# Kernel optimization log

Hardware: AMD Instinct MI355X
Metric: run time of the kernel (lower is better)

## Reference

```python
import jax, jax.numpy as jnp
import numpy as np

ALPHA = 0.5  # trapezoidal_alpha

def rmsnorm(x, w, eps=1e-5):
    return x * jax.lax.rsqrt(jnp.mean(x * x, axis=-1, keepdims=True) + eps) * w

def ssd_scan(x, Bc, Cc, dt, A, alpha):
    # x: (B,L,H,P), Bc/Cc: (B,L,N), dt: (B,L,H), A: (H,)
    da = jnp.exp(dt * A)  # (B,L,H), A < 0 so da in (0,1)
    shift = lambda t: jnp.concatenate([jnp.zeros_like(t[:, :1]), t[:, :-1]], axis=1)
    xp, bp, dtp = shift(x), shift(Bc), shift(dt)
    to_t = lambda t: jnp.moveaxis(t, 1, 0)
    xs = tuple(map(to_t, (x, Bc, Cc, dt, da, xp, bp, dtp)))
    Bb, _, H, P = x.shape
    N = Bc.shape[-1]
    h0 = jnp.zeros((Bb, H, P, N), x.dtype)
    def step(h, inp):
        xt, bt, ct, dtt, dat, xpt, bpt, dtpt = inp
        u = dtt[:, :, None, None] * xt[..., None] * bt[:, None, None, :]      # (B,H,P,N)
        up = dtpt[:, :, None, None] * xpt[..., None] * bpt[:, None, None, :]  # prev input term
        h = dat[:, :, None, None] * (h + alpha * up) + (1.0 - alpha) * u      # trapezoidal update
        y = jnp.einsum('bhpn,bn->bhp', h, ct)
        return h, y
    _, ys = jax.lax.scan(step, h0, xs)
    return jnp.moveaxis(ys, 0, 1)  # (B,L,H,P)

def setup_inputs() -> dict:
    key = jax.random.key(0)
    ks = jax.random.split(key, 10)
    B, NV, NQ = 4, 256, 32
    D, DI, H, N, E, NL = 1024, 2048, 32, 128, 1536, 12
    PROJ = 2 * DI + 2 * N + H  # z | x | B | C | dt
    s = 0.02
    return {
        'visual_tokens': jax.random.normal(ks[0], (B, NV, D), jnp.float32),
        'query_embeds': jax.random.normal(ks[1], (B, NQ, D), jnp.float32),
        'vis_w': jax.random.normal(ks[2], (D, D), jnp.float32) * s,
        'vis_b': jnp.zeros((D,), jnp.float32),
        'qry_w': jax.random.normal(ks[3], (D, D), jnp.float32) * s,
        'qry_b': jnp.zeros((D,), jnp.float32),
        'norm_ws': jnp.ones((NL, D), jnp.float32),
        'in_ws': jax.random.normal(ks[4], (NL, D, PROJ), jnp.float32) * s,
        'dt_biases': jax.random.normal(ks[5], (NL, H), jnp.float32) * 0.5,
        'A_logs': jnp.log(jnp.tile(jnp.arange(1.0, H + 1.0, dtype=jnp.float32)[None], (NL, 1))),
        'D_ssm': jnp.ones((NL, H), jnp.float32),
        'gnorm_ws': jnp.ones((NL, DI), jnp.float32),
        'out_ws': jax.random.normal(ks[6], (NL, DI, D), jnp.float32) * s,
        'norm_f_w': jnp.ones((D,), jnp.float32),
        'head_w': jax.random.normal(ks[7], (D, E), jnp.float32) * s,
        'head_b': jnp.zeros((E,), jnp.float32),
    }

def reference(visual_tokens, query_embeds, vis_w, vis_b, qry_w, qry_b, norm_ws, in_ws,
              dt_biases, A_logs, D_ssm, gnorm_ws, out_ws, norm_f_w, head_w, head_b):
    vis = visual_tokens @ vis_w + vis_b
    qry = query_embeds @ qry_w + qry_b
    hidden = jnp.concatenate([vis, qry], axis=1)  # (B,L,D)
    n_layers = in_ws.shape[0]
    d_inner = gnorm_ws.shape[-1]
    H = A_logs.shape[-1]
    P = d_inner // H
    N = (in_ws.shape[-1] - 2 * d_inner - H) // 2
    for i in range(n_layers):
        res = hidden
        xin = rmsnorm(hidden, norm_ws[i])
        proj = xin @ in_ws[i]  # (B,L,2*DI+2*N+H)
        z = proj[..., :d_inner]
        xss = proj[..., d_inner:2 * d_inner]
        Bc = proj[..., 2 * d_inner:2 * d_inner + N]
        Cc = proj[..., 2 * d_inner + N:2 * d_inner + 2 * N]
        dt = jax.nn.softplus(proj[..., 2 * d_inner + 2 * N:] + dt_biases[i])
        A = -jnp.exp(A_logs[i])
        xr = xss.reshape(xss.shape[0], xss.shape[1], H, P)
        y = ssd_scan(xr, Bc, Cc, dt, A, ALPHA) + D_ssm[i][None, None, :, None] * xr
        y = y.reshape(xss.shape)
        y = rmsnorm(y * jax.nn.silu(z), gnorm_ws[i])  # gated RMSNorm
        hidden = res + y @ out_ws[i]
    hidden = rmsnorm(hidden, norm_f_w)
    pooled = hidden.mean(axis=1)                   # (B,D)
    out = pooled @ head_w + head_b                 # (B,E)
    nrm = jnp.linalg.norm(out, axis=-1, keepdims=True)
    return out / jnp.maximum(nrm, 1e-12)           # F.normalize semantics
```

## Files before the change

kernel.cpp:

```cpp
#include <hip/hip_runtime.h>
#include <cmath>

#define Bb   4
#define Tt   288
#define Dd   1024
#define DIi  2048
#define HH   32
#define PP   64
#define NNs  128
#define PROJ  4384
#define PROJP 4480
#define NLl  12
#define EE   1536

typedef __bf16 bf16x8 __attribute__((ext_vector_type(8)));
typedef float f32x4 __attribute__((ext_vector_type(4)));
typedef float f32x16 __attribute__((ext_vector_type(16)));

__device__ __forceinline__ unsigned short f2bf(float v) {
  __bf16 b = (__bf16)v;
  return __builtin_bit_cast(unsigned short, b);
}
__device__ __forceinline__ float bf2f(unsigned short u) {
  unsigned int x = ((unsigned int)u) << 16;
  return __builtin_bit_cast(float, x);
}
__device__ __forceinline__ void split2(float v, unsigned short& h, unsigned short& l) {
  h = f2bf(v);
  l = f2bf(v - bf2f(h));
}

__device__ __forceinline__ void async16(const void* g, void* l) {
  __builtin_amdgcn_global_load_lds(
      (const __attribute__((address_space(1))) unsigned int*)g,
      (__attribute__((address_space(3))) unsigned int*)l, 16, 0, 0);
}

__device__ inline float block_reduce_sum(float v, float* lds) {
#pragma unroll
  for (int d = 32; d > 0; d >>= 1) v += __shfl_down(v, d, 64);
  int lane = threadIdx.x & 63;
  int w = threadIdx.x >> 6;
  if (lane == 0) lds[w] = v;
  __syncthreads();
  if (threadIdx.x == 0) {
    float s = lds[0];
    int nw = blockDim.x >> 6;
    for (int i = 1; i < nw; i++) s += lds[i];
    lds[0] = s;
  }
  __syncthreads();
  return lds[0];
}

__global__ __launch_bounds__(256) void cvt_act_k(const float* __restrict__ vis,
                                                 const float* __restrict__ qry,
                                                 unsigned short* __restrict__ oh,
                                                 unsigned short* __restrict__ ol) {
  int idx = (blockIdx.x * 256 + threadIdx.x) * 4;
  const float* src = (idx < 1024 * 1024) ? &vis[idx] : &qry[idx - 1024 * 1024];
  float4 v = *(const float4*)src;
  ushort4 h, l;
  split2(v.x, h.x, l.x); split2(v.y, h.y, l.y);
  split2(v.z, h.z, l.z); split2(v.w, h.w, l.w);
  *(ushort4*)&oh[idx] = h;
  *(ushort4*)&ol[idx] = l;
}

__global__ __launch_bounds__(256) void cvt_tr2_k(const float* __restrict__ W,
                                                 unsigned short* __restrict__ Wth,
                                                 unsigned short* __restrict__ Wtl,
                                                 int K, int N,
                                                 size_t wstride, size_t ostride) {
  __shared__ float tile[32][33];
  W   += (size_t)blockIdx.z * wstride;
  Wth += (size_t)blockIdx.z * ostride;
  Wtl += (size_t)blockIdx.z * ostride;
  const int n0 = blockIdx.x * 32, k0 = blockIdx.y * 32;
  const int c = threadIdx.x & 31;
  const int r0 = threadIdx.x >> 5;
#pragma unroll
  for (int j = 0; j < 4; j++) {
    int r = r0 + j * 8;
    int n = n0 + c;
    tile[r][c] = (n < N) ? W[(size_t)(k0 + r) * N + n] : 0.f;
  }
  __syncthreads();
  const int nl = threadIdx.x >> 3;
  const int kl = (threadIdx.x & 7) * 4;
  ushort4 h, l;
  split2(tile[kl + 0][nl], h.x, l.x);
  split2(tile[kl + 1][nl], h.y, l.y);
  split2(tile[kl + 2][nl], h.z, l.z);
  split2(tile[kl + 3][nl], h.w, l.w);
  size_t o = (size_t)(n0 + nl) * K + k0 + kl;
  *(ushort4*)&Wth[o] = h;
  *(ushort4*)&Wtl[o] = l;
}

template<int BM, int BN>
__global__ __launch_bounds__(256) void gemm3_k(
    const unsigned short* __restrict__ Ah, const unsigned short* __restrict__ Al,
    const unsigned short* __restrict__ Wh, const unsigned short* __restrict__ Wl,
    const float* __restrict__ bias, const float* __restrict__ res,
    float* __restrict__ C, int M, int N, int K,
    int rows_per_b, int T_total, int t_off)
{
  constexpr int FM = BM / 64;
  constexpr int FN = BN / 64;
  __shared__ __align__(16) unsigned short Ash[BM * 32];
  __shared__ __align__(16) unsigned short Asl[BM * 32];
  __shared__ __align__(16) unsigned short Bsh[BN * 32];
  __shared__ __align__(16) unsigned short Bsl[BN * 32];
  const int tid = threadIdx.x;
  const int lane = tid & 63;
  const int wm = (tid >> 6) >> 1;
  const int wn = (tid >> 6) & 1;
  const int m0 = blockIdx.y * BM;
  const int n0 = blockIdx.x * BN;
  const int lrow = lane & 31;
  const int lkb = (lane >> 5) * 8;

  f32x16 acc[FM][FN];
#pragma unroll
  for (int i = 0; i < FM; i++)
#pragma unroll
    for (int j = 0; j < FN; j++) acc[i][j] = (f32x16)0.0f;

  for (int k0 = 0; k0 < K; k0 += 32) {
#pragma unroll
    for (int c = 0; c < BM / 64; c++) {
      int o = (c * 256 + tid) * 16;
      int row = o >> 6;
      int colb = o & 63;
      size_t gb = ((size_t)(m0 + row) * K + k0) * 2 + colb;
      async16((const char*)Ah + gb, (char*)Ash + o);
      async16((const char*)Al + gb, (char*)Asl + o);
    }
#pragma unroll
    for (int c = 0; c < BN / 64; c++) {
      int o = (c * 256 + tid) * 16;
      int row = o >> 6;
      int colb = o & 63;
      size_t gb = ((size_t)(n0 + row) * K + k0) * 2 + colb;
      async16((const char*)Wh + gb, (char*)Bsh + o);
      async16((const char*)Wl + gb, (char*)Bsl + o);
    }
    __syncthreads();

#pragma unroll
    for (int kh = 0; kh < 2; kh++) {
      bf16x8 ah[FM], al[FM], bh[FN], bl[FN];
#pragma unroll
      for (int i = 0; i < FM; i++) {
        int off = (wm * (BM / 2) + i * 32 + lrow) * 32 + kh * 16 + lkb;
        ah[i] = *(const bf16x8*)&Ash[off];
        al[i] = *(const bf16x8*)&Asl[off];
      }
#pragma unroll
      for (int j = 0; j < FN; j++) {
        int off = (wn * (BN / 2) + j * 32 + lrow) * 32 + kh * 16 + lkb;
        bh[j] = *(const bf16x8*)&Bsh[off];
        bl[j] = *(const bf16x8*)&Bsl[off];
      }
#pragma unroll
      for (int i = 0; i < FM; i++)
#pragma unroll
        for (int j = 0; j < FN; j++) {
          acc[i][j] = __builtin_amdgcn_mfma_f32_32x32x16_bf16(ah[i], bh[j], acc[i][j], 0, 0, 0);
          acc[i][j] = __builtin_amdgcn_mfma_f32_32x32x16_bf16(ah[i], bl[j], acc[i][j], 0, 0, 0);
          acc[i][j] = __builtin_amdgcn_mfma_f32_32x32x16_bf16(al[i], bh[j], acc[i][j], 0, 0, 0);
        }
    }
    __syncthreads();
  }

  const int r0 = (lane >> 5) * 4;
#pragma unroll
  for (int i = 0; i < FM; i++) {
#pragma unroll
    for (int j = 0; j < FN; j++) {
      int ncol = n0 + wn * (BN / 2) + j * 32 + lrow;
      float bv = bias ? bias[ncol] : 0.f;
#pragma unroll
      for (int rg = 0; rg < 16; rg++) {
        int m = m0 + wm * (BM / 2) + i * 32 + (rg & 3) + 8 * (rg >> 2) + r0;
        size_t orow;
        if (T_total) {
          int bbv = m / rows_per_b;
          orow = (size_t)bbv * T_total + (m - bbv * rows_per_b) + t_off;
        } else {
          orow = (size_t)m;
        }
        float v = acc[i][j][rg] + bv;
        if (res) v += res[orow * N + ncol];
        C[orow * N + ncol] = v;
      }
    }
  }
}

__global__ __launch_bounds__(256) void gemm_k(
    const float* __restrict__ A, const float* __restrict__ W,
    const float* __restrict__ bias, const float* __restrict__ res,
    float* __restrict__ C, int M, int N, int K,
    int rows_per_b, int T_total, int t_off)
{
  __shared__ float As[16][64];
  __shared__ float Ws[16][64];
  const int tid = threadIdx.x;
  const int tx = tid & 15;
  const int ty = tid >> 4;
  const int m0 = blockIdx.y * 64;
  const int n0 = blockIdx.x * 64;
  float acc[4][4] = {};
  const int ar = tid >> 2;
  const int ac = (tid & 3) << 2;
  const int wr = tid >> 4;
  const int wc = (tid & 15) << 2;

  for (int k0 = 0; k0 < K; k0 += 16) {
    float4 av = {0.f, 0.f, 0.f, 0.f};
    int gr = m0 + ar;
    if (gr < M) av = *(const float4*)&A[(size_t)gr * K + k0 + ac];
    As[ac + 0][ar] = av.x; As[ac + 1][ar] = av.y;
    As[ac + 2][ar] = av.z; As[ac + 3][ar] = av.w;

    float4 wv = {0.f, 0.f, 0.f, 0.f};
    int gc = n0 + wc;
    const float* wp = &W[(size_t)(k0 + wr) * N + gc];
    if (gc + 3 < N) {
      wv = *(const float4*)wp;
    } else {
      if (gc + 0 < N) wv.x = wp[0];
      if (gc + 1 < N) wv.y = wp[1];
      if (gc + 2 < N) wv.z = wp[2];
    }
    *(float4*)&Ws[wr][wc] = wv;
    __syncthreads();
#pragma unroll
    for (int kk = 0; kk < 16; kk++) {
      float4 a4 = *(const float4*)&As[kk][ty << 2];
      float4 b4 = *(const float4*)&Ws[kk][tx << 2];
      float a[4] = {a4.x, a4.y, a4.z, a4.w};
      float b[4] = {b4.x, b4.y, b4.z, b4.w};
#pragma unroll
      for (int i = 0; i < 4; i++)
#pragma unroll
        for (int j = 0; j < 4; j++)
          acc[i][j] = fmaf(a[i], b[j], acc[i][j]);
    }
    __syncthreads();
  }
#pragma unroll
  for (int i = 0; i < 4; i++) {
    int gr = m0 + (ty << 2) + i;
    if (gr >= M) continue;
    int bbv = gr / rows_per_b;
    int tt = gr - bbv * rows_per_b;
    size_t orow = (size_t)bbv * T_total + tt + t_off;
#pragma unroll
    for (int j = 0; j < 4; j++) {
      int gc = n0 + (tx << 2) + j;
      if (gc >= N) continue;
      float v = acc[i][j];
      if (bias) v += bias[gc];
      if (res)  v += res[orow * (size_t)N + gc];
      C[orow * (size_t)N + gc] = v;
    }
  }
}

__global__ __launch_bounds__(256) void rmsnorm_k(
    const float* __restrict__ x, const float* __restrict__ w, float* __restrict__ out)
{
  __shared__ float lds[8];
  const int row = blockIdx.x;
  const float* xr = x + (size_t)row * Dd;
  float4 v = *(const float4*)&xr[threadIdx.x << 2];
  float ss = v.x * v.x + v.y * v.y + v.z * v.z + v.w * v.w;
  ss = block_reduce_sum(ss, lds);
  float sc = rsqrtf(ss * (1.f / Dd) + 1e-5f);
  float4 wv = *(const float4*)&w[threadIdx.x << 2];
  float4 o = {v.x * sc * wv.x, v.y * sc * wv.y, v.z * sc * wv.z, v.w * sc * wv.w};
  *(float4*)&out[(size_t)row * Dd + (threadIdx.x << 2)] = o;
}

__global__ __launch_bounds__(256) void rmsnorm2_k(
    const float* __restrict__ x, const float* __restrict__ w,
    unsigned short* __restrict__ oh, unsigned short* __restrict__ ol)
{
  __shared__ float lds[8];
  const int row = blockIdx.x;
  const float* xr = x + (size_t)row * Dd;
  float4 v = *(const float4*)&xr[threadIdx.x << 2];
  float ss = v.x * v.x + v.y * v.y + v.z * v.z + v.w * v.w;
  ss = block_reduce_sum(ss, lds);
  float sc = rsqrtf(ss * (1.f / Dd) + 1e-5f);
  float4 wv = *(const float4*)&w[threadIdx.x << 2];
  ushort4 h, l;
  split2(v.x * sc * wv.x, h.x, l.x);
  split2(v.y * sc * wv.y, h.y, l.y);
  split2(v.z * sc * wv.z, h.z, l.z);
  split2(v.w * sc * wv.w, h.w, l.w);
  size_t o = (size_t)row * Dd + (threadIdx.x << 2);
  *(ushort4*)&oh[o] = h;
  *(ushort4*)&ol[o] = l;
}

__global__ __launch_bounds__(64) void dtcum_k(
    const float* __restrict__ proj, const float* __restrict__ dt_bias,
    const float* __restrict__ A_log,
    float* __restrict__ dtt, double* __restrict__ dcum)
{
  const int h = blockIdx.x & 31;
  const int b = blockIdx.x >> 5;
  const int lane = threadIdx.x;
  const float A = -expf(A_log[h]);
  const float bias = dt_bias[h];
  const int rowo = (b * HH + h) * Tt;
  double base = 0.0;
  for (int c = 0; c < (Tt + 63) / 64; c++) {
    int t = c * 64 + lane;
    float dt = 0.f;
    if (t < Tt) {
      float v = proj[(size_t)(b * Tt + t) * PROJP + 2 * DIi + 2 * NNs + h] + bias;
      dt = (v > 20.f) ? v : log1pf(expf(v));
    }
    double a = (double)(dt * A);
#pragma unroll
    for (int d = 1; d < 64; d <<= 1) {
      double o = __shfl_up(a, d, 64);
      if (lane >= d) a += o;
    }
    double cum = base + a;
    if (t < Tt) { dtt[rowo + t] = dt; dcum[rowo + t] = cum; }
    base = __shfl(cum, 63, 64);
  }
}

__global__ __launch_bounds__(256) void cbgemm_k(const float* __restrict__ proj,
                                                float* __restrict__ St)
{
  const int tI = blockIdx.x, jI = blockIdx.y, b = blockIdx.z;
  if (jI > tI) return;
  __shared__ float Ct[32][130];
  __shared__ float Bt[32][130];
  const int tid = threadIdx.x;
  const int r = tid >> 3;
  const int q = (tid & 7) * 16;
  const float* pb = proj + (size_t)b * Tt * PROJP;
  {
    const float* crow = pb + (size_t)(tI * 32 + r) * PROJP + 2 * DIi + NNs + q;
    const float* brow = pb + (size_t)(jI * 32 + r) * PROJP + 2 * DIi + q;
#pragma unroll
    for (int f = 0; f < 16; f += 4) {
      float4 c4 = *(const float4*)&crow[f];
      float4 b4 = *(const float4*)&brow[f];
      *(float2*)&Ct[r][q + f]     = make_float2(c4.x, c4.y);
      *(float2*)&Ct[r][q + f + 2] = make_float2(c4.z, c4.w);
      *(float2*)&Bt[r][q + f]     = make_float2(b4.x, b4.y);
      *(float2*)&Bt[r][q + f + 2] = make_float2(b4.z, b4.w);
    }
  }
  __syncthreads();
  const int j_r = tid >> 3;
  const int t_c = (tid & 7) * 4;
  float acc[4] = {0.f, 0.f, 0.f, 0.f};
  for (int n = 0; n < NNs; n += 2) {
    float2 b2 = *(const float2*)&Bt[j_r][n];
#pragma unroll
    for (int k = 0; k < 4; k++) {
      float2 c2 = *(const float2*)&Ct[t_c + k][n];
      acc[k] = fmaf(b2.x, c2.x, acc[k]);
      acc[k] = fmaf(b2.y, c2.y, acc[k]);
    }
  }
  float* so = St + ((size_t)b * Tt + jI * 32 + j_r) * Tt + tI * 32 + t_c;
  *(float4*)so = make_float4(acc[0], acc[1], acc[2], acc[3]);
}

__global__ __launch_bounds__(256) void ssd_y_k(
    const float* __restrict__ proj, const float* __restrict__ St,
    const float* __restrict__ dtt, const double* __restrict__ dcum,
    const float* __restrict__ Dssm, float* __restrict__ ybuf)
{
  const int tI = blockIdx.x;
  const int h  = blockIdx.y;
  const int b  = blockIdx.z;
  __shared__ __align__(16) float Xs[32][64];
  __shared__ __align__(16) float Ss[32][36];
  __shared__ double cjs[32];
  const int tid = threadIdx.x;
  const int t_l = tid & 31;
  const int pg  = tid >> 5;
  const int t0  = tI * 32;
  const int rowo = (b * HH + h) * Tt;
  const double ct = dcum[rowo + t0 + t_l];
  const float Ds = Dssm[h];
  const float* pb = proj + (size_t)b * Tt * PROJP;
  float y[8] = {0,0,0,0,0,0,0,0};
  const int sr = tid >> 3;
  const int sq = tid & 7;

  for (int jI = 0; jI <= tI; jI++) {
    const int j0 = jI * 32;
    {
      const float* xr = pb + (size_t)(j0 + sr) * PROJP + DIi + h * PP + sq * 8;
      *(float4*)&Xs[sr][sq * 8]     = *(const float4*)&xr[0];
      *(float4*)&Xs[sr][sq * 8 + 4] = *(const float4*)&xr[4];
    }
    {
      const float* srow = St + ((size_t)b * Tt + j0 + sr) * Tt + t0 + sq * 4;
      float4 s4 = *(const float4*)srow;
      float dj = dtt[rowo + j0 + sr];
      s4.x *= dj; s4.y *= dj; s4.z *= dj; s4.w *= dj;
      *(float4*)&Ss[sr][sq * 4] = s4;
    }
    if (tid < 32) cjs[tid] = dcum[rowo + j0 + tid];
    __syncthreads();

    if (jI < tI) {
#pragma unroll 4
      for (int j = 0; j < 32; j++) {
        float d = (float)(ct - cjs[j]);
        float m = Ss[j][t_l] * expf(fminf(d, 0.f));
        const float* xp = &Xs[j][pg * 8];
        float4 a0 = *(const float4*)&xp[0];
        float4 a1 = *(const float4*)&xp[4];
        y[0] = fmaf(m, a0.x, y[0]); y[1] = fmaf(m, a0.y, y[1]);
        y[2] = fmaf(m, a0.z, y[2]); y[3] = fmaf(m, a0.w, y[3]);
        y[4] = fmaf(m, a1.x, y[4]); y[5] = fmaf(m, a1.y, y[5]);
        y[6] = fmaf(m, a1.z, y[6]); y[7] = fmaf(m, a1.w, y[7]);
      }
    } else {
      for (int j = 0; j < 32; j++) {
        float sv = Ss[j][t_l];
        float d = (float)(ct - cjs[j]);
        float m = sv * expf(fminf(d, 0.f));
        if (j == t_l) m = 0.5f * sv + Ds;
        if (j > t_l)  m = 0.f;
        const float* xp = &Xs[j][pg * 8];
        float4 a0 = *(const float4*)&xp[0];
        float4 a1 = *(const float4*)&xp[4];
        y[0] = fmaf(m, a0.x, y[0]); y[1] = fmaf(m, a0.y, y[1]);
        y[2] = fmaf(m, a0.z, y[2]); y[3] = fmaf(m, a0.w, y[3]);
        y[4] = fmaf(m, a1.x, y[4]); y[5] = fmaf(m, a1.y, y[5]);
        y[6] = fmaf(m, a1.z, y[6]); y[7] = fmaf(m, a1.w, y[7]);
      }
    }
    __syncthreads();
  }
  float* yo = &ybuf[(size_t)(b * Tt + t0 + t_l) * DIi + h * PP + pg * 8];
  *(float4*)&yo[0] = make_float4(y[0], y[1], y[2], y[3]);
  *(float4*)&yo[4] = make_float4(y[4], y[5], y[6], y[7]);
}

__global__ __launch_bounds__(256) void gate_norm2_k(
    const float* __restrict__ ybuf, const float* __restrict__ proj,
    const float* __restrict__ gw,
    unsigned short* __restrict__ yh, unsigned short* __restrict__ yl)
{
  __shared__ float lds[8];
  const int row = blockIdx.x;
  const float* yr = ybuf + (size_t)row * DIi;
  const float* zr = proj + (size_t)row * PROJP;
  const int base = threadIdx.x << 3;
  float4 z0 = *(const float4*)&zr[base];
  float4 z1 = *(const float4*)&zr[base + 4];
  float4 y0 = *(const float4*)&yr[base];
  float4 y1 = *(const float4*)&yr[base + 4];
  float zz[8] = {z0.x, z0.y, z0.z, z0.w, z1.x, z1.y, z1.z, z1.w};
  float yy[8] = {y0.x, y0.y, y0.z, y0.w, y1.x, y1.y, y1.z, y1.w};
  float g[8];
  float ss = 0.f;
#pragma unroll
  for (int e = 0; e < 8; e++) {
    float s = zz[e] / (1.f + expf(-zz[e]));
    float gv = yy[e] * s;
    g[e] = gv;
    ss += gv * gv;
  }
  ss = block_reduce_sum(ss, lds);
  float sc = rsqrtf(ss * (1.f / DIi) + 1e-5f);
  ushort4 h0, l0, h1, l1;
  split2(g[0] * sc * gw[base + 0], h0.x, l0.x);
  split2(g[1] * sc * gw[base + 1], h0.y, l0.y);
  split2(g[2] * sc * gw[base + 2], h0.z, l0.z);
  split2(g[3] * sc * gw[base + 3], h0.w, l0.w);
  split2(g[4] * sc * gw[base + 4], h1.x, l1.x);
  split2(g[5] * sc * gw[base + 5], h1.y, l1.y);
  split2(g[6] * sc * gw[base + 6], h1.z, l1.z);
  split2(g[7] * sc * gw[base + 7], h1.w, l1.w);
  size_t o = (size_t)row * DIi + base;
  *(ushort4*)&yh[o] = h0; *(ushort4*)&yh[o + 4] = h1;
  *(ushort4*)&yl[o] = l0; *(ushort4*)&yl[o + 4] = l1;
}

__global__ void pool_k(const float* __restrict__ xin, float* __restrict__ pooled) {
  int b = blockIdx.x;
  int d = blockIdx.y * 256 + threadIdx.x;
  const float* base = xin + (size_t)b * Tt * Dd + d;
  float s = 0.f;
  for (int t = 0; t < Tt; t++) s += base[(size_t)t * Dd];
  pooled[b * Dd + d] = s * (1.f / Tt);
}

__global__ __launch_bounds__(256) void l2norm_k(float* __restrict__ out) {
  __shared__ float lds[8];
  const int row = blockIdx.x;
  float* r = out + (size_t)row * EE;
  float v[6];
  float ss = 0.f;
#pragma unroll
  for (int e = 0; e < 6; e++) {
    v[e] = r[(e << 8) + threadIdx.x];
    ss += v[e] * v[e];
  }
  ss = block_reduce_sum(ss, lds);
  float sc = 1.f / fmaxf(sqrtf(ss), 1e-12f);
#pragma unroll
  for (int e = 0; e < 6; e++) r[(e << 8) + threadIdx.x] = v[e] * sc;
}

extern "C" void kernel_launch(void* const* d_in, const int* in_sizes, int n_in,
                              void* d_out, int out_size, void* d_ws, size_t ws_size,
                              hipStream_t stream) {
  (void)in_sizes; (void)n_in; (void)out_size;
  const float* visual   = (const float*)d_in[0];
  const float* query    = (const float*)d_in[1];
  const float* vis_w    = (const float*)d_in[2];
  const float* vis_b    = (const float*)d_in[3];
  const float* qry_w    = (const float*)d_in[4];
  const float* qry_b    = (const float*)d_in[5];
  const float* norm_ws  = (const float*)d_in[6];
  const float* in_ws    = (const float*)d_in[7];
  const float* dt_biases= (const float*)d_in[8];
  const float* A_logs   = (const float*)d_in[9];
  const float* D_ssm    = (const float*)d_in[10];
  const float* gnorm_ws = (const float*)d_in[11];
  const float* out_ws   = (const float*)d_in[12];
  const float* norm_f_w = (const float*)d_in[13];
  const float* head_w   = (const float*)d_in[14];
  const float* head_b   = (const float*)d_in[15];
  float* out = (float*)d_out;

  char* w = (char*)d_ws;
  float*          hidden = (float*)w;          w += (size_t)1152 * 1024 * 4;
  unsigned short* xh     = (unsigned short*)w; w += (size_t)1152 * 1024 * 2;
  unsigned short* xl     = (unsigned short*)w; w += (size_t)1152 * 1024 * 2;
  float*          proj   = (float*)w;          w += (size_t)1152 * PROJP * 4;
  float*          ybuf   = (float*)w;          w += (size_t)1152 * 2048 * 4;
  unsigned short* yh     = (unsigned short*)w; w += (size_t)1152 * 2048 * 2;
  unsigned short* yl     = (unsigned short*)w; w += (size_t)1152 * 2048 * 2;
  float*          dtt    = (float*)w;          w += (size_t)Bb * HH * Tt * 4;
  double*         dcum   = (double*)w;         w += (size_t)Bb * HH * Tt * 8;
  float*          Stb    = (float*)w;          w += (size_t)Bb * Tt * Tt * 4;
  float*          pooled = (float*)w;          w += (size_t)4096 * 4;
  unsigned short* wth    = (unsigned short*)w; w += (size_t)PROJP * 1024 * 2;
  unsigned short* wtl    = (unsigned short*)w; w += (size_t)PROJP * 1024 * 2;

  unsigned short* wtin_h  = (unsigned short*)w; w += (size_t)NLl * PROJP * 1024 * 2;
  unsigned short* wtin_l  = (unsigned short*)w; w += (size_t)NLl * PROJP * 1024 * 2;
  unsigned short* wtout_h = (unsigned short*)w; w += (size_t)NLl * 1024 * 2048 * 2;
  unsigned short* wtout_l = (unsigned short*)w; w += (size_t)NLl * 1024 * 2048 * 2;
  unsigned short* wtv_h   = (unsigned short*)w; w += (size_t)1024 * 1024 * 2;
  unsigned short* wtv_l   = (unsigned short*)w; w += (size_t)1024 * 1024 * 2;
  unsigned short* wtq_h   = (unsigned short*)w; w += (size_t)1024 * 1024 * 2;
  unsigned short* wtq_l   = (unsigned short*)w; w += (size_t)1024 * 1024 * 2;
  const bool batched = ((size_t)(w - (char*)d_ws)) <= ws_size;

  dim3 blk(256);

  cvt_act_k<<<1152, blk, 0, stream>>>(visual, query, xh, xl);

  if (batched) {
    cvt_tr2_k<<<dim3(32, 32, 1), blk, 0, stream>>>(vis_w, wtv_h, wtv_l, 1024, 1024, 0, 0);
    cvt_tr2_k<<<dim3(32, 32, 1), blk, 0, stream>>>(qry_w, wtq_h, wtq_l, 1024, 1024, 0, 0);
    cvt_tr2_k<<<dim3(PROJP / 32, 32, NLl), blk, 0, stream>>>(
        in_ws, wtin_h, wtin_l, Dd, PROJ, (size_t)Dd * PROJ, (size_t)PROJP * 1024);
    cvt_tr2_k<<<dim3(32, 64, NLl), blk, 0, stream>>>(
        out_ws, wtout_h, wtout_l, DIi, Dd, (size_t)DIi * Dd, (size_t)1024 * 2048);
    gemm3_k<64, 64><<<dim3(16, 16), blk, 0, stream>>>(
        xh, xl, wtv_h, wtv_l, vis_b, nullptr, hidden, 1024, 1024, 1024, 256, Tt, 0);
    gemm3_k<64, 64><<<dim3(16, 2), blk, 0, stream>>>(
        xh + (size_t)1024 * 1024, xl + (size_t)1024 * 1024, wtq_h, wtq_l,
        qry_b, nullptr, hidden, 128, 1024, 1024, 32, Tt, 256);
  } else {
    cvt_tr2_k<<<dim3(32, 32, 1), blk, 0, stream>>>(vis_w, wth, wtl, 1024, 1024, 0, 0);
    gemm3_k<64, 64><<<dim3(16, 16), blk, 0, stream>>>(
        xh, xl, wth, wtl, vis_b, nullptr, hidden, 1024, 1024, 1024, 256, Tt, 0);
    cvt_tr2_k<<<dim3(32, 32, 1), blk, 0, stream>>>(qry_w, wth, wtl, 1024, 1024, 0, 0);
    gemm3_k<64, 64><<<dim3(16, 2), blk, 0, stream>>>(
        xh + (size_t)1024 * 1024, xl + (size_t)1024 * 1024, wth, wtl,
        qry_b, nullptr, hidden, 128, 1024, 1024, 32, Tt, 256);
  }

  for (int i = 0; i < NLl; i++) {
    rmsnorm2_k<<<Bb * Tt, blk, 0, stream>>>(hidden, norm_ws + i * Dd, xh, xl);
    const unsigned short *bih, *bil;
    if (batched) {
      bih = wtin_h + (size_t)i * PROJP * 1024;
      bil = wtin_l + (size_t)i * PROJP * 1024;
    } else {
      cvt_tr2_k<<<dim3(PROJP / 32, 32, 1), blk, 0, stream>>>(
          in_ws + (size_t)i * Dd * PROJ, wth, wtl, Dd, PROJ, 0, 0);
      bih = wth; bil = wtl;
    }
    gemm3_k<128, 128><<<dim3(PROJP / 128, 9), blk, 0, stream>>>(
        xh, xl, bih, bil, nullptr, nullptr, proj, 1152, PROJP, Dd, 1152, 0, 0);
    dtcum_k<<<Bb * HH, dim3(64), 0, stream>>>(proj, dt_biases + i * HH,
                                              A_logs + i * HH, dtt, dcum);
    cbgemm_k<<<dim3(9, 9, Bb), blk, 0, stream>>>(proj, Stb);
    ssd_y_k<<<dim3(9, HH, Bb), blk, 0, stream>>>(proj, Stb, dtt, dcum,
                                                 D_ssm + i * HH, ybuf);
    gate_norm2_k<<<Bb * Tt, blk, 0, stream>>>(ybuf, proj, gnorm_ws + i * DIi, yh, yl);
    const unsigned short *boh, *bol;
    if (batched) {
      boh = wtout_h + (size_t)i * 1024 * 2048;
      bol = wtout_l + (size_t)i * 1024 * 2048;
    } else {
      cvt_tr2_k<<<dim3(32, 64, 1), blk, 0, stream>>>(
          out_ws + (size_t)i * DIi * Dd, wth, wtl, DIi, Dd, 0, 0);
      boh = wth; bol = wtl;
    }
    gemm3_k<64, 64><<<dim3(16, 18), blk, 0, stream>>>(
        yh, yl, boh, bol, nullptr, hidden, hidden, 1152, Dd, DIi, 1152, 0, 0);
  }

  rmsnorm_k<<<Bb * Tt, blk, 0, stream>>>(hidden, norm_f_w, ybuf);
  pool_k<<<dim3(Bb, 4), blk, 0, stream>>>(ybuf, pooled);
  gemm_k<<<dim3(24, 1), blk, 0, stream>>>(pooled, head_w, head_b, nullptr, out,
                                          Bb, EE, Dd, Bb, 0, 0);
  l2norm_k<<<Bb, blk, 0, stream>>>(out);
}
```

Measured before the change: 2.935 ms.

## Store GEMM operands in MFMA-fragment-packed tile layout

The producer kernels (activation conversion, weight transpose, rmsnorm, gated norm) now write bf16 hi/lo operands in a 32x32 tile-packed layout that matches the MFMA fragment order. The GEMM loads each 32-row by 32-k tile as one contiguous 2KB chunk and reads LDS fragments with lane-linear offsets. This is meant to remove strided global loads and LDS bank conflicts on the fragment reads. It requires every producer and consumer to agree on the layout and assumes dimensions are multiples of 32. Rows written 8 elements at a time with o+4 depend on k alignment within the packing.

```diff
diff --git a/kernel.cpp b/kernel.cpp
--- a/kernel.cpp
+++ b/kernel.cpp
@@ -30,6 +30,13 @@
   l = f2bf(v - bf2f(h));
 }
 
+__device__ __forceinline__ size_t packed_off(int row, int k, int K) {
+  size_t tile = (size_t)(row >> 5) * (K >> 5) + (k >> 5);
+  int half = (k >> 4) & 1;
+  int lane = (row & 31) + (((k >> 3) & 1) << 5);
+  return tile * 1024 + half * 512 + lane * 8 + (k & 7);
+}
+
 __device__ __forceinline__ void async16(const void* g, void* l) {
   __builtin_amdgcn_global_load_lds(
       (const __attribute__((address_space(1))) unsigned int*)g,
@@ -63,8 +70,9 @@
   ushort4 h, l;
   split2(v.x, h.x, l.x); split2(v.y, h.y, l.y);
   split2(v.z, h.z, l.z); split2(v.w, h.w, l.w);
-  *(ushort4*)&oh[idx] = h;
-  *(ushort4*)&ol[idx] = l;
+  size_t po = packed_off(idx >> 10, idx & 1023, 1024);
+  *(ushort4*)&oh[po] = h;
+  *(ushort4*)&ol[po] = l;
 }
 
 __global__ __launch_bounds__(256) void cvt_tr2_k(const float* __restrict__ W,
@@ -93,7 +101,7 @@
   split2(tile[kl + 1][nl], h.y, l.y);
   split2(tile[kl + 2][nl], h.z, l.z);
   split2(tile[kl + 3][nl], h.w, l.w);
-  size_t o = (size_t)(n0 + nl) * K + k0 + kl;
+  size_t o = packed_off(n0 + nl, k0 + kl, K);
   *(ushort4*)&Wth[o] = h;
   *(ushort4*)&Wtl[o] = l;
 }
@@ -119,7 +127,7 @@
   const int m0 = blockIdx.y * BM;
   const int n0 = blockIdx.x * BN;
   const int lrow = lane & 31;
-  const int lkb = (lane >> 5) * 8;
+  const int kb32 = K >> 5;
 
   f32x16 acc[FM][FN];
 #pragma unroll
@@ -127,22 +135,20 @@
 #pragma unroll
     for (int j = 0; j < FN; j++) acc[i][j] = (f32x16)0.0f;
 
-  for (int k0 = 0; k0 < K; k0 += 32) {
+  for (int kb = 0; kb < kb32; kb++) {
 #pragma unroll
     for (int c = 0; c < BM / 64; c++) {
       int o = (c * 256 + tid) * 16;
-      int row = o >> 6;
-      int colb = o & 63;
-      size_t gb = ((size_t)(m0 + row) * K + k0) * 2 + colb;
+      int t = o >> 11;
+      size_t gb = (((size_t)((m0 >> 5) + t) * kb32 + kb) << 11) + (o & 2047);
       async16((const char*)Ah + gb, (char*)Ash + o);
       async16((const char*)Al + gb, (char*)Asl + o);
     }
 #pragma unroll
     for (int c = 0; c < BN / 64; c++) {
       int o = (c * 256 + tid) * 16;
-      int row = o >> 6;
-      int colb = o & 63;
-      size_t gb = ((size_t)(n0 + row) * K + k0) * 2 + colb;
+      int t = o >> 11;
+      size_t gb = (((size_t)((n0 >> 5) + t) * kb32 + kb) << 11) + (o & 2047);
       async16((const char*)Wh + gb, (char*)Bsh + o);
       async16((const char*)Wl + gb, (char*)Bsl + o);
     }
@@ -153,13 +159,13 @@
       bf16x8 ah[FM], al[FM], bh[FN], bl[FN];
 #pragma unroll
       for (int i = 0; i < FM; i++) {
-        int off = (wm * (BM / 2) + i * 32 + lrow) * 32 + kh * 16 + lkb;
+        int off = (wm * FM + i) * 1024 + kh * 512 + lane * 8;
         ah[i] = *(const bf16x8*)&Ash[off];
         al[i] = *(const bf16x8*)&Asl[off];
       }
 #pragma unroll
       for (int j = 0; j < FN; j++) {
-        int off = (wn * (BN / 2) + j * 32 + lrow) * 32 + kh * 16 + lkb;
+        int off = (wn * FN + j) * 1024 + kh * 512 + lane * 8;
         bh[j] = *(const bf16x8*)&Bsh[off];
         bl[j] = *(const bf16x8*)&Bsl[off];
       }
@@ -303,7 +309,7 @@
   split2(v.y * sc * wv.y, h.y, l.y);
   split2(v.z * sc * wv.z, h.z, l.z);
   split2(v.w * sc * wv.w, h.w, l.w);
-  size_t o = (size_t)row * Dd + (threadIdx.x << 2);
+  size_t o = packed_off(row, threadIdx.x << 2, 1024);
   *(ushort4*)&oh[o] = h;
   *(ushort4*)&ol[o] = l;
 }
@@ -492,7 +498,7 @@
   split2(g[5] * sc * gw[base + 5], h1.y, l1.y);
   split2(g[6] * sc * gw[base + 6], h1.z, l1.z);
   split2(g[7] * sc * gw[base + 7], h1.w, l1.w);
-  size_t o = (size_t)row * DIi + base;
+  size_t o = packed_off(row, base, 2048);
   *(ushort4*)&yh[o] = h0; *(ushort4*)&yh[o + 4] = h1;
   *(ushort4*)&yl[o] = l0; *(ushort4*)&yl[o + 4] = l1;
 }
```

After: 2.930 ms. Within noise of the previous version (-0.2%).
